# Optimization experiments

Hardware: AMD Instinct MI355X
Metric: run time of the kernel (lower is better)

## Reference

```python
import jax, jax.numpy as jnp
import numpy as np

B, S, D, HD, P = 4, 8192, 1024, 128, 32
EPS_LN = 1e-5

def setup_inputs() -> dict:
    key = jax.random.key(0)
    ks = jax.random.split(key, 12)
    x      = jax.random.normal(ks[0], (B, S, D), dtype=jnp.float32)
    W_proj = jax.random.normal(ks[1], (8, D, HD), dtype=jnp.float32) * 0.02
    freqs  = jax.random.normal(ks[2], (8, HD), dtype=jnp.float32) * 0.01
    W_pol  = jax.random.normal(ks[3], (8, HD, P), dtype=jnp.float32) * 0.05
    b_pol  = jnp.zeros((8, P), jnp.float32)
    W_imp1 = jax.random.normal(ks[4], (1, 16), dtype=jnp.float32) * 0.5
    b_imp1 = jnp.zeros((16,), jnp.float32)
    W_imp2 = jax.random.normal(ks[5], (16, 1), dtype=jnp.float32) * 0.5
    b_imp2 = jnp.zeros((1,), jnp.float32)
    W_out  = jax.random.normal(ks[6], (D, D), dtype=jnp.float32) * 0.02
    b_out  = jnp.zeros((D,), jnp.float32)
    gamma  = jnp.ones((D,), jnp.float32)
    beta   = jnp.zeros((D,), jnp.float32)
    return dict(x=x, W_proj=W_proj, freqs=freqs, W_pol=W_pol, b_pol=b_pol,
                W_imp1=W_imp1, b_imp1=b_imp1, W_imp2=W_imp2, b_imp2=b_imp2,
                W_out=W_out, b_out=b_out, gamma=gamma, beta=beta)

def reference(x, W_proj, freqs, W_pol, b_pol, W_imp1, b_imp1, W_imp2, b_imp2,
              W_out, b_out, gamma, beta):
    # heads[i] = (x @ W_proj[i]) * cos(pi * freqs[i])   -> (8, B, S, HD)
    heads = jnp.einsum('bsd,hde->hbse', x, W_proj) * jnp.cos(freqs * jnp.pi)[:, None, None, :]

    # --- GuaXiangDuiChong: impedance matrix (B, 8, 8) ---
    hm = heads.mean(axis=2)                                   # (8, B, HD)
    pv = jnp.tanh(jnp.einsum('hbd,hdp->bhp', hm, W_pol) + b_pol[None])  # (B, 8, P)
    pm = pv / jnp.maximum(jnp.linalg.norm(pv, axis=-1, keepdims=True), 1e-12)
    dp = jnp.einsum('bhp,bgp->bhg', pm, pm)                   # (B, 8, 8)
    z = jax.nn.gelu(dp[..., None] * W_imp1[0] + b_imp1, approximate=False)  # (B,8,8,16)
    imp = jax.nn.softplus(jnp.einsum('bhgk,ko->bhgo', z, W_imp2)[..., 0] + b_imp2[0])
    imp = imp * (1.0 - jnp.eye(8, dtype=imp.dtype))           # zero diagonal

    # --- head mixing. Causal masked-mean collapses to row scale (s+1)/S ---
    coeff = (0.1 / (1.0 + imp)) * (1.0 - jnp.eye(8, dtype=imp.dtype))  # (B,8,8), j!=i
    mix = jnp.einsum('big,gbsd->ibsd', coeff, heads)          # (8, B, S, HD)
    causal_scale = (jnp.arange(S, dtype=x.dtype) + 1.0) / S   # (S,)
    out_heads = heads + causal_scale[None, None, :, None] * mix

    merged = out_heads.transpose(1, 2, 0, 3).reshape(B, S, D)
    proj = jnp.einsum('bsd,de->bse', merged, W_out) + b_out   # dropout = identity (eval)
    y = proj + x
    mu = y.mean(axis=-1, keepdims=True)
    var = y.var(axis=-1, keepdims=True)
    y = (y - mu) * jax.lax.rsqrt(var + EPS_LN) * gamma + beta
    return y, imp
```

## Files before the change

kernel.cpp:

```cpp
#include <hip/hip_runtime.h>
#include <hip/hip_bf16.h>
#include <math.h>

typedef __bf16 bf16;
typedef __bf16 bf16x2 __attribute__((ext_vector_type(2)));
typedef __bf16 bf16x4 __attribute__((ext_vector_type(4)));
typedef __bf16 bf16x8 __attribute__((ext_vector_type(8)));
typedef float  f32x4  __attribute__((ext_vector_type(4)));

#define NB 4
#define SS 8192
#define DD 1024
#define MM 32768
#define KK 1024
#define NN 1024
#define NT 16
#define PI_F 3.14159265358979323846f

__device__ __forceinline__ void gl2lds16(const bf16* g, bf16* l) {
    __builtin_amdgcn_global_load_lds(
        (const __attribute__((address_space(1))) void*)g,
        (__attribute__((address_space(3))) void*)l, 16, 0, 0);
}

__global__ __launch_bounds__(256) void prep_all(const float* __restrict__ x,
                                                bf16* __restrict__ xb,
                                                const float* __restrict__ W_proj,
                                                const float* __restrict__ freqs,
                                                const float* __restrict__ W_out,
                                                bf16* __restrict__ WbT1,
                                                bf16* __restrict__ WoT,
                                                float* __restrict__ hm) {
    int blk = blockIdx.x;
    if (blk < MM) {
        size_t i = (size_t)blk * 1024 + threadIdx.x * 4;
        float4 v = *(const float4*)&x[i];
        bf16x4 o;
        o[0] = (bf16)v.x; o[1] = (bf16)v.y; o[2] = (bf16)v.z; o[3] = (bf16)v.w;
        *(bf16x4*)&xb[i] = o;
    } else {
        int idx = (blk - MM) * 256 + threadIdx.x;
        int n = idx >> 10, k = idx & 1023;
        int h = n >> 7, d = n & 127;
        float c = cosf(PI_F * freqs[n]);
        WbT1[idx] = (bf16)(W_proj[(size_t)h * (DD * 128) + (size_t)k * 128 + d] * c);
        WoT[idx]  = (bf16)(W_out[(size_t)k * DD + n]);
        if (idx < NB * DD) hm[idx] = 0.0f;
    }
}

#define SCHED0 __builtin_amdgcn_sched_barrier(0)
#define BAR    SCHED0; __builtin_amdgcn_s_barrier(); SCHED0
#define LGKM0  asm volatile("s_waitcnt lgkmcnt(0)" ::: "memory"); SCHED0

#define STG(g0, g1, uk, ldsBase)                                  \
    gl2lds16((g0) + (uk), &sm[(ldsBase) + w * 512]);              \
    gl2lds16((g1) + (uk), &sm[(ldsBase) + 4096 + w * 512]);

#define READ_A2(MQ, ab)                                                          \
    _Pragma("unroll") for (int m_ = 0; m_ < 4; ++m_) {                           \
        a[m_ * 2 + 0] = *(const bf16x8*)&sm[(ab) + aoff0 + ((MQ)*64 + m_*16)*64];\
        a[m_ * 2 + 1] = *(const bf16x8*)&sm[(ab) + aoff1 + ((MQ)*64 + m_*16)*64];\
    }
#define READ_B2(NQ, bfr, bb)                                                     \
    _Pragma("unroll") for (int n_ = 0; n_ < 2; ++n_) {                           \
        bfr[n_ * 2 + 0] = *(const bf16x8*)&sm[(bb) + boff0 + ((NQ)*32 + n_*16)*64];\
        bfr[n_ * 2 + 1] = *(const bf16x8*)&sm[(bb) + boff1 + ((NQ)*32 + n_*16)*64];\
    }

#define MFMA_Q(MQ, NQ, bfr)                                                    \
    _Pragma("unroll") for (int m_ = 0; m_ < 4; ++m_)                           \
    _Pragma("unroll") for (int n_ = 0; n_ < 2; ++n_)                           \
    _Pragma("unroll") for (int ks_ = 0; ks_ < 2; ++ks_)                        \
        acc[(MQ) * 4 + m_][(NQ) * 2 + n_] =                                    \
            __builtin_amdgcn_mfma_f32_16x16x32_bf16(                           \
                a[m_ * 2 + ks_], bfr[n_ * 2 + ks_],                            \
                acc[(MQ) * 4 + m_][(NQ) * 2 + n_], 0, 0, 0);

template <int MODE>
__global__ __launch_bounds__(512, 2)
void gemm256(const bf16* __restrict__ A, int lda, const bf16* __restrict__ Bt,
             bf16* __restrict__ Cstr, const bf16* __restrict__ residb,
             const float* __restrict__ bias, float* __restrict__ hm) {
    __shared__ bf16 sm[65536];
    const int tid = threadIdx.x;
    const int lane = tid & 63, w = tid >> 6;
    const int wr = w >> 2, wc = w & 3;
    const int l15 = lane & 15, l4 = lane >> 4;

    int wg = blockIdx.x;
    int swz = (wg & 7) * 64 + (wg >> 3);
    const int mt = swz >> 2, ntile = swz & 3;
    const int row0 = mt * 256, col0 = ntile * 256;

    const int aoff0 = (wr * 128 + l15) * 64 + ((l4 ^ (l15 & 7)) << 3);
    const int aoff1 = aoff0 ^ 32;
    const int boff0 = (wc * 64 + l15) * 64 + ((l4 ^ (l15 & 7)) << 3);
    const int boff1 = boff0 ^ 32;

    const int srow = tid >> 3;
    const int scb  = (tid & 7) ^ (srow & 7);
    const bf16* gA00 = A + (size_t)(row0 + srow) * lda + scb * 8;
    const bf16* gA01 = gA00 + (size_t)64 * lda;
    const bf16* gA10 = gA00 + (size_t)128 * lda;
    const bf16* gA11 = gA00 + (size_t)192 * lda;
    const bf16* gB00 = Bt + (size_t)(col0 + srow) * 1024 + scb * 8;
    const bf16* gB01 = gB00 + 64 * 1024;
    const bf16* gB10 = gB00 + 128 * 1024;
    const bf16* gB11 = gB00 + 192 * 1024;

    f32x4 acc[8][4] = {};
    bf16x8 a[8], blo[4], bhi[4];

    STG(gB00, gB01, 0,  32768);
    STG(gB10, gB11, 0,  32768 + 8192);
    STG(gA00, gA01, 0,  0);
    STG(gA10, gA11, 0,  8192);
    STG(gB00, gB01, 64, 49152);
    STG(gB10, gB11, 64, 49152 + 8192);
    asm volatile("s_waitcnt vmcnt(4)" ::: "memory");
    BAR;
    READ_A2(0, 0);
    READ_B2(0, blo, 32768);
    SCHED0;

#pragma unroll 2
    for (int u = 0; u < NT; ++u) {
        const int bo = (u & 1) * 16384;
        const int ab = bo, bb = 32768 + bo;
        const int an = 16384 - bo, bn = 32768 + (16384 - bo);
        const int uk1 = (u + 1) * 64, uk2 = (u + 2) * 64;

        BAR;
        if (u + 1 < NT) { STG(gA00, gA01, uk1, an); }
        LGKM0;
        __builtin_amdgcn_s_setprio(1);
        MFMA_Q(0, 0, blo);
        READ_B2(1, bhi, bb);
        __builtin_amdgcn_s_setprio(0);
        SCHED0;

        BAR;
        if (u + 1 < NT) { STG(gA10, gA11, uk1, an + 8192); }
        LGKM0;
        __builtin_amdgcn_s_setprio(1);
        MFMA_Q(0, 1, bhi);
        READ_A2(1, ab);
        __builtin_amdgcn_s_setprio(0);
        SCHED0;

        BAR;
        if (u + 2 < NT) { STG(gB00, gB01, uk2, bb); }
        LGKM0;
        __builtin_amdgcn_s_setprio(1);
        MFMA_Q(1, 1, bhi);
        __builtin_amdgcn_s_setprio(0);
        if (u + 2 < NT) { asm volatile("s_waitcnt vmcnt(2)" ::: "memory"); }
        else            { asm volatile("s_waitcnt vmcnt(0)" ::: "memory"); }
        SCHED0;

        BAR;
        if (u + 2 < NT) { STG(gB10, gB11, uk2, bb + 8192); }
        __builtin_amdgcn_s_setprio(1);
        MFMA_Q(1, 0, blo);
        if (u + 1 < NT) {
            READ_A2(0, an);
            READ_B2(0, blo, bn);
        }
        __builtin_amdgcn_s_setprio(0);
        SCHED0;
    }

    if (MODE == 0) {
        const int batch = row0 >> 13;
#pragma unroll
        for (int mg = 0; mg < 8; ++mg) {
            int rbase = row0 + wr * 128 + (mg >> 2) * 64 + (mg & 3) * 16 + l4 * 4;
#pragma unroll
            for (int j = 0; j < 4; ++j) {
                size_t row = rbase + j;
#pragma unroll
                for (int ng = 0; ng < 4; ++ng) {
                    int col = col0 + wc * 64 + ng * 16 + l15;
                    Cstr[row * 2048 + col] = (bf16)acc[mg][ng][j];
                }
            }
        }
#pragma unroll
        for (int ng = 0; ng < 4; ++ng) {
            float s = 0;
#pragma unroll
            for (int mg = 0; mg < 8; ++mg)
#pragma unroll
                for (int j = 0; j < 4; ++j) s += acc[mg][ng][j];
            int col = col0 + wc * 64 + ng * 16 + l15;
            atomicAdd(&hm[batch * DD + col], s);
        }
    } else {
        float bi[4];
#pragma unroll
        for (int ng = 0; ng < 4; ++ng) bi[ng] = bias[col0 + wc * 64 + ng * 16 + l15];
#pragma unroll
        for (int mg = 0; mg < 8; ++mg) {
            int rbase = row0 + wr * 128 + (mg >> 2) * 64 + (mg & 3) * 16 + l4 * 4;
#pragma unroll
            for (int j = 0; j < 4; ++j) {
                size_t row = rbase + j;
#pragma unroll
                for (int ng = 0; ng < 4; ++ng) {
                    int col = col0 + wc * 64 + ng * 16 + l15;
                    Cstr[row * 2048 + col] =
                        (bf16)(acc[mg][ng][j] + bi[ng] + (float)residb[row * 1024 + col]);
                }
            }
        }
    }
}

__global__ __launch_bounds__(1024) void imp_k(const float* __restrict__ hm,
                                              const float* __restrict__ W_pol,
                                              const float* __restrict__ b_pol,
                                              const float* __restrict__ W_imp1,
                                              const float* __restrict__ b_imp1,
                                              const float* __restrict__ W_imp2,
                                              const float* __restrict__ b_imp2,
                                              float* __restrict__ imp_out,
                                              float* __restrict__ coeff) {
    __shared__ float pm_s[32][32];
    int tid = threadIdx.x;
    int bh = tid >> 5, p = tid & 31;
    int b = bh >> 3, h = bh & 7;
    float a = b_pol[h * 32 + p];
    for (int d = 0; d < 128; ++d)
        a += hm[b * DD + h * 128 + d] * (1.0f / SS) * W_pol[(h * 128 + d) * 32 + p];
    float pv = tanhf(a);
    pm_s[bh][p] = pv;
    __syncthreads();
    float ss = 0;
    for (int q = 0; q < 32; ++q) ss += pm_s[bh][q] * pm_s[bh][q];
    float pmv = pv / fmaxf(sqrtf(ss), 1e-12f);
    __syncthreads();
    pm_s[bh][p] = pmv;
    __syncthreads();
    if (tid < 256) {
        int b2 = tid >> 6, h2 = (tid >> 3) & 7, g = tid & 7;
        float dp = 0;
        for (int q = 0; q < 32; ++q) dp += pm_s[b2 * 8 + h2][q] * pm_s[b2 * 8 + g][q];
        float a2 = 0;
        for (int k = 0; k < 16; ++k) {
            float zin = dp * W_imp1[k] + b_imp1[k];
            float zg = 0.5f * zin * (1.0f + erff(zin * 0.70710678118654752f));
            a2 += zg * W_imp2[k];
        }
        float spin = a2 + b_imp2[0];
        float impv = (spin > 20.0f) ? spin : log1pf(expf(spin));
        if (h2 == g) impv = 0.0f;
        imp_out[tid] = impv;
        coeff[tid] = (h2 == g) ? 0.0f : 0.1f / (1.0f + impv);
    }
}

__global__ __launch_bounds__(256) void mix_k(const char* __restrict__ slots,
                                             const float* __restrict__ coeff,
                                             char* __restrict__ slots_w) {
    __shared__ float cf[64];
    int tid = threadIdx.x;
    size_t r0 = (size_t)blockIdx.x * 4;
    int b = (int)(r0 >> 13);
    if (tid < 64) cf[tid] = coeff[b * 64 + tid];
    __syncthreads();
    int lr = tid >> 6;
    int d2 = tid & 63;
    size_t r = r0 + lr;
    int s = (int)(r & (SS - 1));
    float cs = (float)(s + 1) * (1.0f / SS);
    const bf16* hrow = (const bf16*)(slots + r * 4096);
    bf16* mrow = (bf16*)(slots_w + r * 4096 + 2048);
    float v0[8], v1[8];
#pragma unroll
    for (int g = 0; g < 8; ++g) {
        bf16x2 v = *(const bf16x2*)&hrow[g * 128 + d2 * 2];
        v0[g] = (float)v[0]; v1[g] = (float)v[1];
    }
#pragma unroll
    for (int h = 0; h < 8; ++h) {
        float a0 = 0, a1 = 0;
#pragma unroll
        for (int g = 0; g < 8; ++g) {
            float c = cf[h * 8 + g];
            a0 += c * v0[g]; a1 += c * v1[g];
        }
        bf16x2 o;
        o[0] = (bf16)(v0[h] + cs * a0);
        o[1] = (bf16)(v1[h] + cs * a1);
        *(bf16x2*)&mrow[h * 128 + d2 * 2] = o;
    }
}

__global__ __launch_bounds__(256) void ln_k(char* __restrict__ slots,
                                            const float* __restrict__ gamma,
                                            const float* __restrict__ beta) {
    size_t r = blockIdx.x;
    int tid = threadIdx.x;
    const bf16* zrow = (const bf16*)(slots + r * 4096);
    float* yrow = (float*)(slots + r * 4096);
    int e0 = tid * 4;
    bf16x4 zv = *(const bf16x4*)&zrow[e0];
    float vx = (float)zv[0], vy = (float)zv[1], vz = (float)zv[2], vw = (float)zv[3];
    float sum = vx + vy + vz + vw;
    float sq  = vx * vx + vy * vy + vz * vz + vw * vw;
    for (int off = 32; off > 0; off >>= 1) {
        sum += __shfl_down(sum, off);
        sq  += __shfl_down(sq, off);
    }
    __shared__ float red[8];
    int lane = tid & 63, wv = tid >> 6;
    if (lane == 0) { red[wv] = sum; red[4 + wv] = sq; }
    __syncthreads();
    float tot = red[0] + red[1] + red[2] + red[3];
    float tsq = red[4] + red[5] + red[6] + red[7];
    float mu  = tot * (1.0f / DD);
    float var = tsq * (1.0f / DD) - mu * mu;
    float rs  = rsqrtf(var + 1e-5f);
    float4 g4 = *(const float4*)&gamma[e0];
    float4 b4 = *(const float4*)&beta[e0];
    float4 o;
    o.x = (vx - mu) * rs * g4.x + b4.x;
    o.y = (vy - mu) * rs * g4.y + b4.y;
    o.z = (vz - mu) * rs * g4.z + b4.z;
    o.w = (vw - mu) * rs * g4.w + b4.w;
    *(float4*)&yrow[e0] = o;
}

extern "C" void kernel_launch(void* const* d_in, const int* in_sizes, int n_in,
                              void* d_out, int out_size, void* d_ws, size_t ws_size,
                              hipStream_t stream) {
    const float* x      = (const float*)d_in[0];
    const float* W_proj = (const float*)d_in[1];
    const float* freqs  = (const float*)d_in[2];
    const float* W_pol  = (const float*)d_in[3];
    const float* b_pol  = (const float*)d_in[4];
    const float* W_imp1 = (const float*)d_in[5];
    const float* b_imp1 = (const float*)d_in[6];
    const float* W_imp2 = (const float*)d_in[7];
    const float* b_imp2 = (const float*)d_in[8];
    const float* W_out  = (const float*)d_in[9];
    const float* b_out  = (const float*)d_in[10];
    const float* gamma  = (const float*)d_in[11];
    const float* beta   = (const float*)d_in[12];

    char* ws = (char*)d_ws;
    bf16* xb     = (bf16*)ws;
    bf16* WbT1   = (bf16*)(ws + ((size_t)64 << 20));
    bf16* WoT    = (bf16*)(ws + ((size_t)66 << 20));
    float* hm    = (float*)(ws + ((size_t)68 << 20));
    float* coeff = (float*)(ws + ((size_t)68 << 20) + 16384);

    char* slots = (char*)d_out;
    float* imp_out = (float*)d_out + (size_t)MM * DD;

    prep_all<<<MM + 4096, 256, 0, stream>>>(x, xb, W_proj, freqs, W_out,
                                            WbT1, WoT, hm);

    gemm256<0><<<512, 512, 0, stream>>>(xb, 1024, WbT1, (bf16*)slots,
                                        nullptr, nullptr, hm);

    imp_k<<<1, 1024, 0, stream>>>(hm, W_pol, b_pol, W_imp1, b_imp1, W_imp2, b_imp2,
                                  imp_out, coeff);

    mix_k<<<MM / 4, 256, 0, stream>>>(slots, coeff, slots);

    gemm256<1><<<512, 512, 0, stream>>>((const bf16*)slots + 1024, 2048, WoT,
                                        (bf16*)slots, xb, b_out, nullptr);

    ln_k<<<MM, 256, 0, stream>>>(slots, gamma, beta);
}
```

Baseline: 269.9 us.

## Replace 256x256 GEMM tile with 128x256 tile and triple-buffered K=32 pipeline

```diff
diff --git a/kernel.cpp b/kernel.cpp
--- a/kernel.cpp
+++ b/kernel.cpp
@@ -14,7 +14,7 @@
 #define MM 32768
 #define KK 1024
 #define NN 1024
-#define NT 16
+#define NTK 32
 #define PI_F 3.14159265358979323846f
 
 __device__ __forceinline__ void gl2lds16(const bf16* g, bf16* l) {
@@ -49,168 +49,147 @@
     }
 }
 
+
 #define SCHED0 __builtin_amdgcn_sched_barrier(0)
 #define BAR    SCHED0; __builtin_amdgcn_s_barrier(); SCHED0
 #define LGKM0  asm volatile("s_waitcnt lgkmcnt(0)" ::: "memory"); SCHED0
 
-#define STG(g0, g1, uk, ldsBase)                                  \
-    gl2lds16((g0) + (uk), &sm[(ldsBase) + w * 512]);              \
-    gl2lds16((g1) + (uk), &sm[(ldsBase) + 4096 + w * 512]);
-
-#define READ_A2(MQ, ab)                                                          \
-    _Pragma("unroll") for (int m_ = 0; m_ < 4; ++m_) {                           \
-        a[m_ * 2 + 0] = *(const bf16x8*)&sm[(ab) + aoff0 + ((MQ)*64 + m_*16)*64];\
-        a[m_ * 2 + 1] = *(const bf16x8*)&sm[(ab) + aoff1 + ((MQ)*64 + m_*16)*64];\
-    }
-#define READ_B2(NQ, bfr, bb)                                                     \
-    _Pragma("unroll") for (int n_ = 0; n_ < 2; ++n_) {                           \
-        bfr[n_ * 2 + 0] = *(const bf16x8*)&sm[(bb) + boff0 + ((NQ)*32 + n_*16)*64];\
-        bfr[n_ * 2 + 1] = *(const bf16x8*)&sm[(bb) + boff1 + ((NQ)*32 + n_*16)*64];\
-    }
-
-#define MFMA_Q(MQ, NQ, bfr)                                                    \
-    _Pragma("unroll") for (int m_ = 0; m_ < 4; ++m_)                           \
-    _Pragma("unroll") for (int n_ = 0; n_ < 2; ++n_)                           \
-    _Pragma("unroll") for (int ks_ = 0; ks_ < 2; ++ks_)                        \
-        acc[(MQ) * 4 + m_][(NQ) * 2 + n_] =                                    \
-            __builtin_amdgcn_mfma_f32_16x16x32_bf16(                           \
-                a[m_ * 2 + ks_], bfr[n_ * 2 + ks_],                            \
-                acc[(MQ) * 4 + m_][(NQ) * 2 + n_], 0, 0, 0);
+#define RD_A(dst, off)                                                        \
+    _Pragma("unroll") for (int m_ = 0; m_ < 4; ++m_)                          \
+        dst[m_] = *(const bf16x8*)&sm[(off) + a_lane + m_ * 512];
+
+#define RD_B(dst, off)                                                        \
+    _Pragma("unroll") for (int n_ = 0; n_ < 4; ++n_)                          \
+        dst[n_] = *(const bf16x8*)&sm[(off) + b_lane + n_ * 512];
+
+#define MFMA_P(af, BR)                                                        \
+    _Pragma("unroll") for (int m_ = 0; m_ < 4; ++m_)                          \
+    _Pragma("unroll") for (int n_ = 0; n_ < 4; ++n_)                          \
+        acc[(BR) + m_][n_] = __builtin_amdgcn_mfma_f32_16x16x32_bf16(         \
+            af[m_], bc[n_], acc[(BR) + m_][n_], 0, 0, 0);
+
+#define STG_A(U, AB)                                                          \
+    gl2lds16(gA0 + (U) * 32, &sm[(AB) * 4096 + wv512]);                       \
+    gl2lds16(gA1 + (U) * 32, &sm[(AB) * 4096 + 2048 + wv512]);
+
+#define STG_B(U, BB)                                                          \
+    gl2lds16(gB0 + (U) * 32, &sm[12288 + (BB) * 8192 + wv512]);               \
+    gl2lds16(gB1 + (U) * 32, &sm[12288 + (BB) * 8192 + 2048 + wv512]);        \
+    gl2lds16(gB2 + (U) * 32, &sm[12288 + (BB) * 8192 + 4096 + wv512]);        \
+    gl2lds16(gB3 + (U) * 32, &sm[12288 + (BB) * 8192 + 6144 + wv512]);
+
+#define KSTEP(U, ACUR, AN2, ANX, BCUR, STG, RD)                               \
+    {                                                                         \
+        BAR;                                                                  \
+        if (STG) { STG_A((U) + 2, AN2); }                                     \
+        LGKM0;                                                                \
+        __builtin_amdgcn_s_setprio(1);                                        \
+        MFMA_P(af0, 0);                                                       \
+        RD_A(af1, (ACUR) * 4096 + 2048);                                      \
+        __builtin_amdgcn_s_setprio(0);                                        \
+        if (STG) { asm volatile("s_waitcnt vmcnt(2)" ::: "memory"); }         \
+        else     { asm volatile("s_waitcnt vmcnt(0)" ::: "memory"); }         \
+        SCHED0;                                                               \
+        BAR;                                                                  \
+        if (STG) { STG_B((U) + 2, (BCUR)); }                                  \
+        LGKM0;                                                                \
+        __builtin_amdgcn_s_setprio(1);                                        \
+        MFMA_P(af1, 4);                                                       \
+        if (RD) { RD_A(af0, (ANX) * 4096);                                    \
+                  RD_B(bc, 12288 + (1 - (BCUR)) * 8192); }                    \
+        __builtin_amdgcn_s_setprio(0);                                        \
+        SCHED0;                                                               \
+    }
 
 template <int MODE>
-__global__ __launch_bounds__(512, 2)
-void gemm256(const bf16* __restrict__ A, int lda, const bf16* __restrict__ Bt,
+__global__ __launch_bounds__(256, 2)
+void gemm128(const bf16* __restrict__ A, int lda, const bf16* __restrict__ Bt,
              bf16* __restrict__ Cstr, const bf16* __restrict__ residb,
              const float* __restrict__ bias, float* __restrict__ hm) {
-    __shared__ bf16 sm[65536];
+    __shared__ bf16 sm[28672];
     const int tid = threadIdx.x;
     const int lane = tid & 63, w = tid >> 6;
-    const int wr = w >> 2, wc = w & 3;
     const int l15 = lane & 15, l4 = lane >> 4;
-
-    int wg = blockIdx.x;
-    int swz = (wg & 7) * 64 + (wg >> 3);
-    const int mt = swz >> 2, ntile = swz & 3;
-    const int row0 = mt * 256, col0 = ntile * 256;
-
-    const int aoff0 = (wr * 128 + l15) * 64 + ((l4 ^ (l15 & 7)) << 3);
-    const int aoff1 = aoff0 ^ 32;
-    const int boff0 = (wc * 64 + l15) * 64 + ((l4 ^ (l15 & 7)) << 3);
-    const int boff1 = boff0 ^ 32;
-
-    const int srow = tid >> 3;
-    const int scb  = (tid & 7) ^ (srow & 7);
-    const bf16* gA00 = A + (size_t)(row0 + srow) * lda + scb * 8;
-    const bf16* gA01 = gA00 + (size_t)64 * lda;
-    const bf16* gA10 = gA00 + (size_t)128 * lda;
-    const bf16* gA11 = gA00 + (size_t)192 * lda;
-    const bf16* gB00 = Bt + (size_t)(col0 + srow) * 1024 + scb * 8;
-    const bf16* gB01 = gB00 + 64 * 1024;
-    const bf16* gB10 = gB00 + 128 * 1024;
-    const bf16* gB11 = gB00 + 192 * 1024;
+    const int wv512 = w * 512;
+
+    int orig = blockIdx.x;
+    int xcd = orig & 7, k = orig >> 3;
+    const int mt = xcd * 32 + (k >> 2);
+    const int nt = k & 3;
+    const int row0 = mt * 128, col0 = nt * 256;
+
+    const int aq = ((l4 ^ ((l15 >> 1) & 3)) << 3);
+    const int a_lane = l15 * 32 + aq;
+    const int b_lane = w * 2048 + l15 * 32 + aq;
+
+    const int srow = tid >> 2;
+    const int sq = (tid & 3) ^ ((tid >> 3) & 3);
+    const bf16* gA0 = A + (size_t)(row0 + srow) * lda + sq * 8;
+    const bf16* gA1 = gA0 + (size_t)64 * lda;
+    const bf16* gB0 = Bt + (size_t)(col0 + srow) * 1024 + sq * 8;
+    const bf16* gB1 = gB0 + 64 * 1024;
+    const bf16* gB2 = gB0 + 128 * 1024;
+    const bf16* gB3 = gB0 + 192 * 1024;
 
     f32x4 acc[8][4] = {};
-    bf16x8 a[8], blo[4], bhi[4];
-
-    STG(gB00, gB01, 0,  32768);
-    STG(gB10, gB11, 0,  32768 + 8192);
-    STG(gA00, gA01, 0,  0);
-    STG(gA10, gA11, 0,  8192);
-    STG(gB00, gB01, 64, 49152);
-    STG(gB10, gB11, 64, 49152 + 8192);
-    asm volatile("s_waitcnt vmcnt(4)" ::: "memory");
+    bf16x8 af0[4], af1[4], bc[4];
+
+    STG_A(0, 0); STG_B(0, 0); STG_A(1, 1); STG_B(1, 1);
+    asm volatile("s_waitcnt vmcnt(6)" ::: "memory");
     BAR;
-    READ_A2(0, 0);
-    READ_B2(0, blo, 32768);
+    RD_A(af0, 0);
+    RD_B(bc, 12288);
     SCHED0;
 
-#pragma unroll 2
-    for (int u = 0; u < NT; ++u) {
-        const int bo = (u & 1) * 16384;
-        const int ab = bo, bb = 32768 + bo;
-        const int an = 16384 - bo, bn = 32768 + (16384 - bo);
-        const int uk1 = (u + 1) * 64, uk2 = (u + 2) * 64;
-
-        BAR;
-        if (u + 1 < NT) { STG(gA00, gA01, uk1, an); }
-        LGKM0;
-        __builtin_amdgcn_s_setprio(1);
-        MFMA_Q(0, 0, blo);
-        READ_B2(1, bhi, bb);
-        __builtin_amdgcn_s_setprio(0);
-        SCHED0;
-
-        BAR;
-        if (u + 1 < NT) { STG(gA10, gA11, uk1, an + 8192); }
-        LGKM0;
-        __builtin_amdgcn_s_setprio(1);
-        MFMA_Q(0, 1, bhi);
-        READ_A2(1, ab);
-        __builtin_amdgcn_s_setprio(0);
-        SCHED0;
-
-        BAR;
-        if (u + 2 < NT) { STG(gB00, gB01, uk2, bb); }
-        LGKM0;
-        __builtin_amdgcn_s_setprio(1);
-        MFMA_Q(1, 1, bhi);
-        __builtin_amdgcn_s_setprio(0);
-        if (u + 2 < NT) { asm volatile("s_waitcnt vmcnt(2)" ::: "memory"); }
-        else            { asm volatile("s_waitcnt vmcnt(0)" ::: "memory"); }
-        SCHED0;
-
-        BAR;
-        if (u + 2 < NT) { STG(gB10, gB11, uk2, bb + 8192); }
-        __builtin_amdgcn_s_setprio(1);
-        MFMA_Q(1, 0, blo);
-        if (u + 1 < NT) {
-            READ_A2(0, an);
-            READ_B2(0, blo, bn);
-        }
-        __builtin_amdgcn_s_setprio(0);
-        SCHED0;
-    }
+    for (int uu = 0; uu < 30; uu += 6) {
+#pragma unroll
+        for (int v = 0; v < 6; ++v) {
+            KSTEP(uu + v, (v) % 3, (v + 2) % 3, (v + 1) % 3, (v & 1), true, true);
+        }
+    }
+    KSTEP(30, 0, 2, 1, 0, false, true);
+    KSTEP(31, 1, 0, 2, 1, false, false);
 
     if (MODE == 0) {
         const int batch = row0 >> 13;
 #pragma unroll
-        for (int mg = 0; mg < 8; ++mg) {
-            int rbase = row0 + wr * 128 + (mg >> 2) * 64 + (mg & 3) * 16 + l4 * 4;
+        for (int mf = 0; mf < 8; ++mf) {
+            int rbase = row0 + mf * 16 + l4 * 4;
 #pragma unroll
             for (int j = 0; j < 4; ++j) {
                 size_t row = rbase + j;
 #pragma unroll
-                for (int ng = 0; ng < 4; ++ng) {
-                    int col = col0 + wc * 64 + ng * 16 + l15;
-                    Cstr[row * 2048 + col] = (bf16)acc[mg][ng][j];
+                for (int nf = 0; nf < 4; ++nf) {
+                    int col = col0 + w * 64 + nf * 16 + l15;
+                    Cstr[row * 2048 + col] = (bf16)acc[mf][nf][j];
                 }
             }
         }
 #pragma unroll
-        for (int ng = 0; ng < 4; ++ng) {
+        for (int nf = 0; nf < 4; ++nf) {
             float s = 0;
 #pragma unroll
-            for (int mg = 0; mg < 8; ++mg)
-#pragma unroll
-                for (int j = 0; j < 4; ++j) s += acc[mg][ng][j];
-            int col = col0 + wc * 64 + ng * 16 + l15;
+            for (int mf = 0; mf < 8; ++mf)
+#pragma unroll
+                for (int j = 0; j < 4; ++j) s += acc[mf][nf][j];
+            int col = col0 + w * 64 + nf * 16 + l15;
             atomicAdd(&hm[batch * DD + col], s);
         }
     } else {
         float bi[4];
 #pragma unroll
-        for (int ng = 0; ng < 4; ++ng) bi[ng] = bias[col0 + wc * 64 + ng * 16 + l15];
-#pragma unroll
-        for (int mg = 0; mg < 8; ++mg) {
-            int rbase = row0 + wr * 128 + (mg >> 2) * 64 + (mg & 3) * 16 + l4 * 4;
+        for (int nf = 0; nf < 4; ++nf) bi[nf] = bias[col0 + w * 64 + nf * 16 + l15];
+#pragma unroll
+        for (int mf = 0; mf < 8; ++mf) {
+            int rbase = row0 + mf * 16 + l4 * 4;
 #pragma unroll
             for (int j = 0; j < 4; ++j) {
                 size_t row = rbase + j;
 #pragma unroll
-                for (int ng = 0; ng < 4; ++ng) {
-                    int col = col0 + wc * 64 + ng * 16 + l15;
+                for (int nf = 0; nf < 4; ++nf) {
+                    int col = col0 + w * 64 + nf * 16 + l15;
                     Cstr[row * 2048 + col] =
-                        (bf16)(acc[mg][ng][j] + bi[ng] + (float)residb[row * 1024 + col]);
+                        (bf16)(acc[mf][nf][j] + bi[nf] + (float)residb[row * 1024 + col]);
                 }
             }
         }
@@ -247,10 +226,10 @@
         float dp = 0;
         for (int q = 0; q < 32; ++q) dp += pm_s[b2 * 8 + h2][q] * pm_s[b2 * 8 + g][q];
         float a2 = 0;
-        for (int k = 0; k < 16; ++k) {
-            float zin = dp * W_imp1[k] + b_imp1[k];
+        for (int kk = 0; kk < 16; ++kk) {
+            float zin = dp * W_imp1[kk] + b_imp1[kk];
             float zg = 0.5f * zin * (1.0f + erff(zin * 0.70710678118654752f));
-            a2 += zg * W_imp2[k];
+            a2 += zg * W_imp2[kk];
         }
         float spin = a2 + b_imp2[0];
         float impv = (spin > 20.0f) ? spin : log1pf(expf(spin));
@@ -362,16 +341,16 @@
     prep_all<<<MM + 4096, 256, 0, stream>>>(x, xb, W_proj, freqs, W_out,
                                             WbT1, WoT, hm);
 
-    gemm256<0><<<512, 512, 0, stream>>>(xb, 1024, WbT1, (bf16*)slots,
-                                        nullptr, nullptr, hm);
+    gemm128<0><<<1024, 256, 0, stream>>>(xb, 1024, WbT1, (bf16*)slots,
+                                         nullptr, nullptr, hm);
 
     imp_k<<<1, 1024, 0, stream>>>(hm, W_pol, b_pol, W_imp1, b_imp1, W_imp2, b_imp2,
                                   imp_out, coeff);
 
     mix_k<<<MM / 4, 256, 0, stream>>>(slots, coeff, slots);
 
-    gemm256<1><<<512, 512, 0, stream>>>((const bf16*)slots + 1024, 2048, WoT,
-                                        (bf16*)slots, xb, b_out, nullptr);
+    gemm128<1><<<1024, 256, 0, stream>>>((const bf16*)slots + 1024, 2048, WoT,
+                                         (bf16*)slots, xb, b_out, nullptr);
 
     ln_k<<<MM, 256, 0, stream>>>(slots, gamma, beta);
 }
```

Measured after the change: 279.2 us. 1.03x slower.

## Restructure GEMM main loop into two-stage unrolled LDS pipeline with explicit barriers

Applied to the files above, without the earlier changes.

```diff
diff --git a/kernel.cpp b/kernel.cpp
--- a/kernel.cpp
+++ b/kernel.cpp
@@ -14,7 +14,6 @@
 #define MM 32768
 #define KK 1024
 #define NN 1024
-#define NT 16
 #define PI_F 3.14159265358979323846f
 
 __device__ __forceinline__ void gl2lds16(const bf16* g, bf16* l) {
@@ -49,9 +48,14 @@
     }
 }
 
+
 #define SCHED0 __builtin_amdgcn_sched_barrier(0)
 #define BAR    SCHED0; __builtin_amdgcn_s_barrier(); SCHED0
 #define LGKM0  asm volatile("s_waitcnt lgkmcnt(0)" ::: "memory"); SCHED0
+#define PRIO1  __builtin_amdgcn_s_setprio(1)
+#define PRIO0  __builtin_amdgcn_s_setprio(0)
+#define VMC(N) asm volatile("s_waitcnt vmcnt(" #N ")" ::: "memory")
+#define NOPS   ((void)0)
 
 #define STG(g0, g1, uk, ldsBase)                                  \
     gl2lds16((g0) + (uk), &sm[(ldsBase) + w * 512]);              \
@@ -76,6 +80,37 @@
             __builtin_amdgcn_mfma_f32_16x16x32_bf16(                           \
                 a[m_ * 2 + ks_], bfr[n_ * 2 + ks_],                            \
                 acc[(MQ) * 4 + m_][(NQ) * 2 + n_], 0, 0, 0);
+
+#define ITER(uk1, STG3, STG4, STG5, STG6, STG7, STG8, VM4, VM8)                \
+  {                                                  \
+    STG(gA00, gA01, (uk1), 16384);                                             \
+    READ_A2(0, 0); READ_B2(0, blo, 32768);                                     \
+    asm volatile("s_waitcnt lgkmcnt(8)" ::: "memory");                         \
+    BAR; LGKM0; PRIO1; MFMA_Q(0, 0, blo); PRIO0; BAR;                          \
+                                                            \
+    STG(gA10, gA11, (uk1), 16384 + 8192);                                      \
+    READ_B2(1, bhi, 32768);                                                    \
+    BAR; LGKM0; PRIO1; MFMA_Q(0, 1, bhi); PRIO0; BAR;                          \
+                                                            \
+    STG3; READ_A2(1, 0);                                                       \
+    BAR; LGKM0; PRIO1; MFMA_Q(1, 1, bhi); PRIO0; BAR;                          \
+                                          \
+    STG4; VM4;                                                                 \
+    BAR; PRIO1; MFMA_Q(1, 0, blo); PRIO0; BAR;                                 \
+                                                   \
+    STG5; READ_A2(0, 16384); READ_B2(0, blo, 49152);                           \
+    asm volatile("s_waitcnt lgkmcnt(8)" ::: "memory");                         \
+    BAR; LGKM0; PRIO1; MFMA_Q(0, 0, blo); PRIO0; BAR;                          \
+                                                            \
+    STG6; READ_B2(1, bhi, 49152);                                              \
+    BAR; LGKM0; PRIO1; MFMA_Q(0, 1, bhi); PRIO0; BAR;                          \
+                                                            \
+    STG7; READ_A2(1, 16384);                                                   \
+    BAR; LGKM0; PRIO1; MFMA_Q(1, 1, bhi); PRIO0; BAR;                          \
+                                          \
+    STG8; VM8;                                                                 \
+    BAR; PRIO1; MFMA_Q(1, 0, blo); PRIO0; BAR;                                 \
+  }
 
 template <int MODE>
 __global__ __launch_bounds__(512, 2)
@@ -112,64 +147,25 @@
     f32x4 acc[8][4] = {};
     bf16x8 a[8], blo[4], bhi[4];
 
-    STG(gB00, gB01, 0,  32768);
-    STG(gB10, gB11, 0,  32768 + 8192);
-    STG(gA00, gA01, 0,  0);
-    STG(gA10, gA11, 0,  8192);
-    STG(gB00, gB01, 64, 49152);
-    STG(gB10, gB11, 64, 49152 + 8192);
-    asm volatile("s_waitcnt vmcnt(4)" ::: "memory");
+    STG(gA00, gA01, 0,  0);     STG(gA10, gA11, 0,  8192);
+    STG(gB00, gB01, 0,  32768); STG(gB10, gB11, 0,  40960);
+    STG(gA00, gA01, 64, 16384); STG(gA10, gA11, 64, 24576);
+    STG(gB00, gB01, 64, 49152); STG(gB10, gB11, 64, 57344);
+    VMC(0);
     BAR;
-    READ_A2(0, 0);
-    READ_B2(0, blo, 32768);
-    SCHED0;
-
-#pragma unroll 2
-    for (int u = 0; u < NT; ++u) {
-        const int bo = (u & 1) * 16384;
-        const int ab = bo, bb = 32768 + bo;
-        const int an = 16384 - bo, bn = 32768 + (16384 - bo);
-        const int uk1 = (u + 1) * 64, uk2 = (u + 2) * 64;
-
-        BAR;
-        if (u + 1 < NT) { STG(gA00, gA01, uk1, an); }
-        LGKM0;
-        __builtin_amdgcn_s_setprio(1);
-        MFMA_Q(0, 0, blo);
-        READ_B2(1, bhi, bb);
-        __builtin_amdgcn_s_setprio(0);
-        SCHED0;
-
-        BAR;
-        if (u + 1 < NT) { STG(gA10, gA11, uk1, an + 8192); }
-        LGKM0;
-        __builtin_amdgcn_s_setprio(1);
-        MFMA_Q(0, 1, bhi);
-        READ_A2(1, ab);
-        __builtin_amdgcn_s_setprio(0);
-        SCHED0;
-
-        BAR;
-        if (u + 2 < NT) { STG(gB00, gB01, uk2, bb); }
-        LGKM0;
-        __builtin_amdgcn_s_setprio(1);
-        MFMA_Q(1, 1, bhi);
-        __builtin_amdgcn_s_setprio(0);
-        if (u + 2 < NT) { asm volatile("s_waitcnt vmcnt(2)" ::: "memory"); }
-        else            { asm volatile("s_waitcnt vmcnt(0)" ::: "memory"); }
-        SCHED0;
-
-        BAR;
-        if (u + 2 < NT) { STG(gB10, gB11, uk2, bb + 8192); }
-        __builtin_amdgcn_s_setprio(1);
-        MFMA_Q(1, 0, blo);
-        if (u + 1 < NT) {
-            READ_A2(0, an);
-            READ_B2(0, blo, bn);
-        }
-        __builtin_amdgcn_s_setprio(0);
-        SCHED0;
-    }
+
+#pragma unroll 1
+    for (int i = 0; i < 7; ++i) {
+        const int uk1 = (2 * i + 1) * 64;
+        const int uk2 = (2 * i + 2) * 64;
+        const int uk3 = (2 * i + 3) * 64;
+        ITER(uk1,
+             STG(gB00, gB01, uk2, 32768), STG(gB10, gB11, uk2, 40960),
+             STG(gA00, gA01, uk2, 0),     STG(gA10, gA11, uk2, 8192),
+             STG(gB00, gB01, uk3, 49152), STG(gB10, gB11, uk3, 57344),
+             VMC(4), VMC(4));
+    }
+    ITER(960, NOPS, NOPS, NOPS, NOPS, NOPS, NOPS, VMC(0), NOPS);
 
     if (MODE == 0) {
         const int batch = row0 >> 13;
@@ -247,10 +243,10 @@
         float dp = 0;
         for (int q = 0; q < 32; ++q) dp += pm_s[b2 * 8 + h2][q] * pm_s[b2 * 8 + g][q];
         float a2 = 0;
-        for (int k = 0; k < 16; ++k) {
-            float zin = dp * W_imp1[k] + b_imp1[k];
+        for (int kk = 0; kk < 16; ++kk) {
+            float zin = dp * W_imp1[kk] + b_imp1[kk];
             float zg = 0.5f * zin * (1.0f + erff(zin * 0.70710678118654752f));
-            a2 += zg * W_imp2[k];
+            a2 += zg * W_imp2[kk];
         }
         float spin = a2 + b_imp2[0];
         float impv = (spin > 20.0f) ? spin : log1pf(expf(spin));
```

Result: slower. 275.6 us (+2.1%).
